# Kernel optimization log

Hardware: AMD Instinct MI355X
Metric: run time of the kernel (lower is better)

## Reference

```python
import jax, jax.numpy as jnp
import numpy as np

LN_EPS = 1e-3  # keras LayerNormalization default epsilon


def _layernorm(x, gamma, beta):
    mu = jnp.mean(x, axis=-1, keepdims=True)
    var = jnp.mean(jnp.square(x - mu), axis=-1, keepdims=True)
    return (x - mu) * jax.lax.rsqrt(var + LN_EPS) * gamma + beta


def setup_inputs() -> dict:
    key = jax.random.key(0)
    ks = jax.random.split(key, 8)
    B, H, W, C = 4, 64, 64, 256
    units = 256
    s = 1.0 / np.sqrt(C)  # he-normal-ish scale for 1x1 convs
    return {
        "inputs": jax.random.normal(ks[0], (B, H, W, C), jnp.float32),
        "context": jax.random.normal(ks[1], (B, H, W, C), jnp.float32),
        "Wq": jax.random.normal(ks[2], (C, units), jnp.float32) * s,
        "bq": jnp.zeros((units,), jnp.float32),
        "Wk": jax.random.normal(ks[3], (C, units), jnp.float32) * s,
        "bk": jnp.zeros((units,), jnp.float32),
        "Wv": jax.random.normal(ks[4], (C, units), jnp.float32) * s,
        "bv": jnp.zeros((units,), jnp.float32),
        "Wp": jax.random.normal(ks[5], (units, units), jnp.float32) * s,
        "bp": jnp.zeros((units,), jnp.float32),
        "gamma": jnp.ones((C,), jnp.float32),
        "beta": jnp.zeros((C,), jnp.float32),
    }


def reference(inputs, context, Wq, bq, Wk, bk, Wv, bv, Wp, bp, gamma, beta):
    B, H, W, C = inputs.shape
    units = Wq.shape[1]
    scale = jnp.float32(units) ** -0.5

    x_n = _layernorm(inputs, gamma, beta)          # normalized inputs (also residual base)
    q = jnp.einsum('bhwc,cu->bhwu', x_n, Wq) + bq   # [B,H,W,U]
    k = jnp.einsum('bhwc,cu->bhwu', context, Wk) + bk
    v = jnp.einsum('bhwc,cu->bhwu', context, Wv) + bv

    # full (h*w) x (H*W) score tensor, as in the original
    scores = jnp.einsum('bhwc,bHWc->bhwHW', q, k) * scale
    scores = scores.reshape(B, H, W, H * W)
    attn = jax.nn.softmax(scores, axis=-1).reshape(B, H, W, H, W)

    out = jnp.einsum('bhwHW,bHWc->bhwc', attn, v)
    proj = jnp.einsum('bhwc,cu->bhwu', out, Wp) + bp
    return x_n + proj
```

## Files before the change

kernel.cpp:

```cpp
#include <hip/hip_runtime.h>

typedef short v8s __attribute__((ext_vector_type(8)));
typedef float v4f __attribute__((ext_vector_type(4)));
using u16 = unsigned short;


__device__ __forceinline__ u16 f2b(float f) {
  union { float f; unsigned u; } v; v.f = f;
  unsigned r = v.u + 0x7FFFu + ((v.u >> 16) & 1u);
  return (u16)(r >> 16);
}

__global__ void ln_prep(const float* __restrict__ x, const float* __restrict__ ctx,
                        const float* __restrict__ gamma, const float* __restrict__ beta,
                        float* __restrict__ xn_f, u16* __restrict__ xn_b,
                        u16* __restrict__ ctx_b)
{
  const int tid = threadIdx.x;
  const int wid = tid >> 6, lane = tid & 63;
  const int row = blockIdx.x * 4 + wid;
  const size_t tidx = ((size_t)(row >> 4) * 8 + (lane >> 3)) * 512 +
                      (((lane >> 1) & 3) * 16 + (row & 15)) * 8 + (lane & 1) * 4;
  if (blockIdx.y == 0) {
    const float4 xv = *(const float4*)(x + (size_t)row * 256 + lane * 4);
    float s1 = xv.x + xv.y + xv.z + xv.w;
    float s2 = xv.x*xv.x + xv.y*xv.y + xv.z*xv.z + xv.w*xv.w;
#pragma unroll
    for (int m = 32; m >= 1; m >>= 1) {
      s1 += __shfl_xor(s1, m);
      s2 += __shfl_xor(s2, m);
    }
    const float mu  = s1 * (1.0f/256.0f);
    const float var = s2 * (1.0f/256.0f) - mu*mu;
    const float rs  = rsqrtf(var + 1e-3f);
    const float4 g = *(const float4*)(gamma + lane*4);
    const float4 b = *(const float4*)(beta  + lane*4);
    float4 y;
    y.x = (xv.x-mu)*rs*g.x + b.x;
    y.y = (xv.y-mu)*rs*g.y + b.y;
    y.z = (xv.z-mu)*rs*g.z + b.z;
    y.w = (xv.w-mu)*rs*g.w + b.w;
    *(float4*)(xn_f + (size_t)row*256 + lane*4) = y;
    ushort4 yb; yb.x=f2b(y.x); yb.y=f2b(y.y); yb.z=f2b(y.z); yb.w=f2b(y.w);
    *(ushort4*)(xn_b + tidx) = yb;
  } else {
    const float4 cv = *(const float4*)(ctx + (size_t)row * 256 + lane * 4);
    ushort4 cb; cb.x=f2b(cv.x); cb.y=f2b(cv.y); cb.z=f2b(cv.z); cb.w=f2b(cv.w);
    *(ushort4*)(ctx_b + tidx) = cb;
  }
}

__global__ void wtrans(const float* __restrict__ wq, const float* __restrict__ wk,
                       const float* __restrict__ wv, const float* __restrict__ wp,
                       u16* __restrict__ tq, u16* __restrict__ tk,
                       u16* __restrict__ tv, u16* __restrict__ tp)
{
  const float* src; u16* dst;
  switch (blockIdx.y) {
    case 0:  src = wq; dst = tq; break;
    case 1:  src = wk; dst = tk; break;
    case 2:  src = wv; dst = tv; break;
    default: src = wp; dst = tp; break;
  }
  const int t  = threadIdx.x;
  const int kk = blockIdx.x * 16 + (t >> 4);
  const int n0 = (t & 15) * 16;
  const size_t base = (size_t)((t & 15) * 8 + (kk >> 5)) * 512 +
                      ((kk >> 3) & 3) * 16 * 8 + (kk & 7);
#pragma unroll
  for (int j = 0; j < 16; j++)
    dst[base + (size_t)j * 8] = f2b(src[(size_t)kk * 256 + n0 + j]);
}

__global__ __launch_bounds__(256) void gemm_qkv(
    const u16* __restrict__ xn_b, const u16* __restrict__ ctx_b,
    const u16* __restrict__ wqt, const u16* __restrict__ wkt, const u16* __restrict__ wvt,
    const float* __restrict__ bq, const float* __restrict__ bk, const float* __restrict__ bv,
    u16* __restrict__ qo, u16* __restrict__ ko, u16* __restrict__ vto)
{
  const int mode = blockIdx.y;
  const u16* A; const u16* Wt; const float* bias;
  if (mode == 0)      { A = xn_b;  Wt = wqt; bias = bq; }
  else if (mode == 1) { A = ctx_b; Wt = wkt; bias = bk; }
  else                { A = ctx_b; Wt = wvt; bias = bv; }
  const int wid = threadIdx.x >> 6, lane = threadIdx.x & 63;
  const int lm = lane & 15, q4 = lane >> 4;
  const int m0 = blockIdx.x * 64 + wid * 16;
  const u16* abase = A + (size_t)(m0 >> 4) * 4096 + lane * 8;
  v8s af[8];
#pragma unroll
  for (int kf = 0; kf < 8; kf++) af[kf] = *(const v8s*)(abase + kf * 512);
#pragma unroll
  for (int ct = 0; ct < 16; ct++) {
    const int c = ct * 16 + lm;
    const u16* wbase = Wt + (size_t)ct * 4096 + lane * 8;
    v4f acc = {0.f, 0.f, 0.f, 0.f};
#pragma unroll
    for (int kf = 0; kf < 8; kf++)
      acc = __builtin_amdgcn_mfma_f32_16x16x32_bf16(af[kf], *(const v8s*)(wbase + kf * 512), acc, 0, 0, 0);
    const float bb = bias[c];
    if (mode == 2) {
      const int b = m0 >> 12;
      const int chunk = (m0 & 4095) >> 6;
      const int kic = (m0 & 63) + q4 * 4;
      const int ks = kic >> 5;
      const int q4p = (kic >> 3) & 3;
      const size_t idx = ((size_t)(b * 64 + chunk) * 32 + (c >> 4) * 2 + ks) * 512 +
                         (q4p * 16 + (c & 15)) * 8 + (q4 & 1) * 4;
      ushort4 pk;
      pk.x = f2b(acc[0] + bb); pk.y = f2b(acc[1] + bb);
      pk.z = f2b(acc[2] + bb); pk.w = f2b(acc[3] + bb);
      *(ushort4*)(vto + idx) = pk;
    } else {
      u16* out = (mode == 0) ? qo : ko;
      const size_t base = ((size_t)(m0 >> 4) * 8 + (c >> 5)) * 512 +
                          (((c >> 3) & 3) * 16 + q4 * 4) * 8 + (c & 7);
#pragma unroll
      for (int r = 0; r < 4; r++)
        out[base + (size_t)r * 8] = f2b(acc[r] + bb);
    }
  }
}

__global__ __launch_bounds__(256, 1) void attn_kernel(
    const u16* __restrict__ q, const u16* __restrict__ k,
    const u16* __restrict__ vt, u16* __restrict__ ao)
{
  __shared__ u16 P[2][64][72];
  __shared__ float Lp[4][64];
  __shared__ float Lt[64];
  const int b   = blockIdx.y;
  const int tid = threadIdx.x;
  const int w   = tid >> 6, lane = tid & 63;
  const int lm  = lane & 15, q4 = lane >> 4;
  const int m0  = blockIdx.x * 64;
  const u16* qb = q  + (size_t)b * 1048576;
  const u16* kb = k  + (size_t)b * 1048576;
  const u16* vb = vt + (size_t)b * 1048576;

  v8s qf[4][8];
#pragma unroll
  for (int qt = 0; qt < 4; qt++) {
    const u16* qbase = qb + (size_t)((m0 >> 4) + qt) * 4096 + lane * 8;
#pragma unroll
    for (int kf = 0; kf < 8; kf++) qf[qt][kf] = *(const v8s*)(qbase + kf * 512);
  }

  v4f o[4][4];
#pragma unroll
  for (int qt = 0; qt < 4; qt++)
#pragma unroll
    for (int ct = 0; ct < 4; ct++) o[qt][ct] = (v4f){0.f, 0.f, 0.f, 0.f};
  float lsum[4] = {0.f, 0.f, 0.f, 0.f};

  v8s kfr[8];
  {
    const u16* kbase = kb + (size_t)(w) * 4096 + lane * 8;
#pragma unroll
    for (int kf = 0; kf < 8; kf++) kfr[kf] = *(const v8s*)(kbase + kf * 512);
  }

  for (int s0 = 0; s0 < 4096; s0 += 64) {
    const int pb = (s0 >> 6) & 1;
    const int chunk = s0 >> 6;
    v8s vfr[4][2];
#pragma unroll
    for (int ct = 0; ct < 4; ct++) {
      const u16* vbase = vb + ((size_t)chunk * 32 + (w * 4 + ct) * 2) * 512 + lane * 8;
      vfr[ct][0] = *(const v8s*)(vbase);
      vfr[ct][1] = *(const v8s*)(vbase + 512);
    }
    v4f sc[4];
#pragma unroll
    for (int qt = 0; qt < 4; qt++) sc[qt] = (v4f){0.f, 0.f, 0.f, 0.f};
#pragma unroll
    for (int kf = 0; kf < 8; kf++)
#pragma unroll
      for (int qt = 0; qt < 4; qt++)
        sc[qt] = __builtin_amdgcn_mfma_f32_16x16x32_bf16(kfr[kf], qf[qt][kf], sc[qt], 0, 0, 0);
    {
      const int sn = (s0 + 64) & 4095;
      const u16* kbase = kb + (size_t)((sn >> 4) + w) * 4096 + lane * 8;
#pragma unroll
      for (int kf = 0; kf < 8; kf++) kfr[kf] = *(const v8s*)(kbase + kf * 512);
    }
#pragma unroll
    for (int qt = 0; qt < 4; qt++) {
      const float e0 = exp2f(sc[qt][0] * 0.09016844f);
      const float e1 = exp2f(sc[qt][1] * 0.09016844f);
      const float e2 = exp2f(sc[qt][2] * 0.09016844f);
      const float e3 = exp2f(sc[qt][3] * 0.09016844f);
      lsum[qt] += (e0 + e1) + (e2 + e3);
      unsigned d0, d1;
      asm("v_cvt_pk_bf16_f32 %0, %1, %2" : "=v"(d0) : "v"(e0), "v"(e1));
      asm("v_cvt_pk_bf16_f32 %0, %1, %2" : "=v"(d1) : "v"(e2), "v"(e3));
      uint2 pk; pk.x = d0; pk.y = d1;
      *(uint2*)(&P[pb][qt * 16 + lm][w * 16 + q4 * 4]) = pk;
    }
    __syncthreads();
#pragma unroll
    for (int qt = 0; qt < 4; qt++) {
      const v8s pf0 = *(const v8s*)(&P[pb][qt * 16 + lm][q4 * 8]);
      const v8s pf1 = *(const v8s*)(&P[pb][qt * 16 + lm][32 + q4 * 8]);
#pragma unroll
      for (int ct = 0; ct < 4; ct++) {
        o[qt][ct] = __builtin_amdgcn_mfma_f32_16x16x32_bf16(pf0, vfr[ct][0], o[qt][ct], 0, 0, 0);
        o[qt][ct] = __builtin_amdgcn_mfma_f32_16x16x32_bf16(pf1, vfr[ct][1], o[qt][ct], 0, 0, 0);
      }
    }
  }

#pragma unroll
  for (int qt = 0; qt < 4; qt++) {
    float t = lsum[qt];
    t += __shfl_xor(t, 16);
    t += __shfl_xor(t, 32);
    lsum[qt] = t;
  }
  if (q4 == 0) {
#pragma unroll
    for (int qt = 0; qt < 4; qt++) Lp[w][qt * 16 + lm] = lsum[qt];
  }
  __syncthreads();
  if (tid < 64) Lt[tid] = Lp[0][tid] + Lp[1][tid] + Lp[2][tid] + Lp[3][tid];
  __syncthreads();

  const int rstrip0 = (b * 4096 + m0) >> 4;
#pragma unroll
  for (int qt = 0; qt < 4; qt++)
#pragma unroll
    for (int r = 0; r < 4; r++) {
      const float linv = 1.0f / Lt[qt * 16 + q4 * 4 + r];
#pragma unroll
      for (int ct = 0; ct < 4; ct++) {
        const int ch = w * 64 + ct * 16 + lm;
        const size_t idx = ((size_t)(rstrip0 + qt) * 8 + (ch >> 5)) * 512 +
                           (((ch >> 3) & 3) * 16 + q4 * 4 + r) * 8 + (ch & 7);
        ao[idx] = f2b(o[qt][ct][r] * linv);
      }
    }
}

__global__ __launch_bounds__(256) void gemm_proj(
    const u16* __restrict__ A, const u16* __restrict__ Wt, const float* __restrict__ bias,
    const float* __restrict__ xn_f, float* __restrict__ out)
{
  const int wid = threadIdx.x >> 6, lane = threadIdx.x & 63;
  const int lm = lane & 15, q4 = lane >> 4;
  const int m0 = blockIdx.x * 64 + wid * 16;
  const u16* abase = A + (size_t)(m0 >> 4) * 4096 + lane * 8;
  v8s af[8];
#pragma unroll
  for (int kf = 0; kf < 8; kf++) af[kf] = *(const v8s*)(abase + kf * 512);
#pragma unroll
  for (int ct = 0; ct < 16; ct++) {
    const int c = ct * 16 + lm;
    const u16* wbase = Wt + (size_t)ct * 4096 + lane * 8;
    v4f acc = {0.f, 0.f, 0.f, 0.f};
#pragma unroll
    for (int kf = 0; kf < 8; kf++)
      acc = __builtin_amdgcn_mfma_f32_16x16x32_bf16(af[kf], *(const v8s*)(wbase + kf * 512), acc, 0, 0, 0);
    const float bb = bias[c];
#pragma unroll
    for (int r = 0; r < 4; r++) {
      const size_t idx = (size_t)(m0 + q4 * 4 + r) * 256 + c;
      out[idx] = xn_f[idx] + acc[r] + bb;
    }
  }
}

extern "C" void kernel_launch(void* const* d_in, const int* in_sizes, int n_in,
                              void* d_out, int out_size, void* d_ws, size_t ws_size,
                              hipStream_t stream)
{
  (void)in_sizes; (void)n_in; (void)out_size; (void)ws_size;
  const float* inputs  = (const float*)d_in[0];
  const float* context = (const float*)d_in[1];
  const float* Wq = (const float*)d_in[2];
  const float* bq = (const float*)d_in[3];
  const float* Wk = (const float*)d_in[4];
  const float* bk = (const float*)d_in[5];
  const float* Wv = (const float*)d_in[6];
  const float* bv = (const float*)d_in[7];
  const float* Wp = (const float*)d_in[8];
  const float* bp = (const float*)d_in[9];
  const float* gamma = (const float*)d_in[10];
  const float* beta  = (const float*)d_in[11];
  float* out = (float*)d_out;

  char* p = (char*)d_ws;
  float* xn_f = (float*)p; p += (size_t)16384 * 256 * 4;
  u16* xn_b   = (u16*)p;   p += (size_t)16384 * 256 * 2;
  u16* ctx_b  = (u16*)p;   p += (size_t)16384 * 256 * 2;
  u16* qbuf   = (u16*)p;   p += (size_t)16384 * 256 * 2;
  u16* kbuf   = (u16*)p;   p += (size_t)16384 * 256 * 2;
  u16* vtbuf  = (u16*)p;   p += (size_t)16384 * 256 * 2;
  u16* wqt = (u16*)p; p += (size_t)256 * 256 * 2;
  u16* wkt = (u16*)p; p += (size_t)256 * 256 * 2;
  u16* wvt = (u16*)p; p += (size_t)256 * 256 * 2;
  u16* wpt = (u16*)p; p += (size_t)256 * 256 * 2;
  u16* aobuf = xn_b;

  ln_prep<<<dim3(4096, 2), 256, 0, stream>>>(inputs, context, gamma, beta, xn_f, xn_b, ctx_b);
  wtrans<<<dim3(16, 4), 256, 0, stream>>>(Wq, Wk, Wv, Wp, wqt, wkt, wvt, wpt);
  gemm_qkv<<<dim3(256, 3), 256, 0, stream>>>(xn_b, ctx_b, wqt, wkt, wvt, bq, bk, bv, qbuf, kbuf, vtbuf);
  attn_kernel<<<dim3(64, 4), 256, 0, stream>>>(qbuf, kbuf, vtbuf, aobuf);
  gemm_proj<<<dim3(256), 256, 0, stream>>>(aobuf, wpt, bp, xn_f, out);
}
```

Baseline: 248.3 us.

## Fold softmax scale into Wq, retile QKV/proj GEMMs, remap attention blocks

Folds the softmax scale (with log2e) into the Q weight and bias, so the attention loop no longer multiplies each score before exp2. The QKV and projection GEMMs are retiled so each wave computes 64 rows and reuses each loaded weight fragment across four row tiles, using 128-thread blocks. The attention grid is flattened and blocks are interleaved across batches, which may change L2 locality for K/V. The __syncthreads in the attention loop is replaced with an explicit LDS waitcnt plus s_barrier. Rounding Q after scaling changes numerics slightly, and the wider per-wave tiles raise register pressure.

```diff
diff --git a/kernel.cpp b/kernel.cpp
--- a/kernel.cpp
+++ b/kernel.cpp
@@ -4,6 +4,7 @@
 typedef float v4f __attribute__((ext_vector_type(4)));
 using u16 = unsigned short;
 
+#define QSCALE 0.09016844f
 
 __device__ __forceinline__ u16 f2b(float f) {
   union { float f; unsigned u; } v; v.f = f;
@@ -55,9 +56,9 @@
                        u16* __restrict__ tq, u16* __restrict__ tk,
                        u16* __restrict__ tv, u16* __restrict__ tp)
 {
-  const float* src; u16* dst;
+  const float* src; u16* dst; float scl = 1.0f;
   switch (blockIdx.y) {
-    case 0:  src = wq; dst = tq; break;
+    case 0:  src = wq; dst = tq; scl = QSCALE; break;
     case 1:  src = wk; dst = tk; break;
     case 2:  src = wv; dst = tv; break;
     default: src = wp; dst = tp; break;
@@ -69,10 +70,10 @@
                       ((kk >> 3) & 3) * 16 * 8 + (kk & 7);
 #pragma unroll
   for (int j = 0; j < 16; j++)
-    dst[base + (size_t)j * 8] = f2b(src[(size_t)kk * 256 + n0 + j]);
-}
-
-__global__ __launch_bounds__(256) void gemm_qkv(
+    dst[base + (size_t)j * 8] = f2b(src[(size_t)kk * 256 + n0 + j] * scl);
+}
+
+__global__ __launch_bounds__(128) void gemm_qkv(
     const u16* __restrict__ xn_b, const u16* __restrict__ ctx_b,
     const u16* __restrict__ wqt, const u16* __restrict__ wkt, const u16* __restrict__ wvt,
     const float* __restrict__ bq, const float* __restrict__ bk, const float* __restrict__ bv,
@@ -83,41 +84,56 @@
   if (mode == 0)      { A = xn_b;  Wt = wqt; bias = bq; }
   else if (mode == 1) { A = ctx_b; Wt = wkt; bias = bk; }
   else                { A = ctx_b; Wt = wvt; bias = bv; }
+  const float bscale = (mode == 0) ? QSCALE : 1.0f;
   const int wid = threadIdx.x >> 6, lane = threadIdx.x & 63;
   const int lm = lane & 15, q4 = lane >> 4;
-  const int m0 = blockIdx.x * 64 + wid * 16;
-  const u16* abase = A + (size_t)(m0 >> 4) * 4096 + lane * 8;
-  v8s af[8];
-#pragma unroll
-  for (int kf = 0; kf < 8; kf++) af[kf] = *(const v8s*)(abase + kf * 512);
+  const int m0 = blockIdx.x * 128 + wid * 64;
+  v8s af[4][8];
+#pragma unroll
+  for (int rt = 0; rt < 4; rt++) {
+    const u16* abase = A + (size_t)((m0 >> 4) + rt) * 4096 + lane * 8;
+#pragma unroll
+    for (int kf = 0; kf < 8; kf++) af[rt][kf] = *(const v8s*)(abase + kf * 512);
+  }
 #pragma unroll
   for (int ct = 0; ct < 16; ct++) {
     const int c = ct * 16 + lm;
     const u16* wbase = Wt + (size_t)ct * 4096 + lane * 8;
-    v4f acc = {0.f, 0.f, 0.f, 0.f};
+    v8s wf[8];
+#pragma unroll
+    for (int kf = 0; kf < 8; kf++) wf[kf] = *(const v8s*)(wbase + kf * 512);
+    v4f acc[4];
+#pragma unroll
+    for (int rt = 0; rt < 4; rt++) acc[rt] = (v4f){0.f, 0.f, 0.f, 0.f};
 #pragma unroll
     for (int kf = 0; kf < 8; kf++)
-      acc = __builtin_amdgcn_mfma_f32_16x16x32_bf16(af[kf], *(const v8s*)(wbase + kf * 512), acc, 0, 0, 0);
-    const float bb = bias[c];
-    if (mode == 2) {
-      const int b = m0 >> 12;
-      const int chunk = (m0 & 4095) >> 6;
-      const int kic = (m0 & 63) + q4 * 4;
-      const int ks = kic >> 5;
-      const int q4p = (kic >> 3) & 3;
-      const size_t idx = ((size_t)(b * 64 + chunk) * 32 + (c >> 4) * 2 + ks) * 512 +
-                         (q4p * 16 + (c & 15)) * 8 + (q4 & 1) * 4;
-      ushort4 pk;
-      pk.x = f2b(acc[0] + bb); pk.y = f2b(acc[1] + bb);
-      pk.z = f2b(acc[2] + bb); pk.w = f2b(acc[3] + bb);
-      *(ushort4*)(vto + idx) = pk;
-    } else {
-      u16* out = (mode == 0) ? qo : ko;
-      const size_t base = ((size_t)(m0 >> 4) * 8 + (c >> 5)) * 512 +
-                          (((c >> 3) & 3) * 16 + q4 * 4) * 8 + (c & 7);
-#pragma unroll
-      for (int r = 0; r < 4; r++)
-        out[base + (size_t)r * 8] = f2b(acc[r] + bb);
+#pragma unroll
+      for (int rt = 0; rt < 4; rt++)
+        acc[rt] = __builtin_amdgcn_mfma_f32_16x16x32_bf16(af[rt][kf], wf[kf], acc[rt], 0, 0, 0);
+    const float bb = bias[c] * bscale;
+#pragma unroll
+    for (int rt = 0; rt < 4; rt++) {
+      const int row16 = m0 + rt * 16;
+      if (mode == 2) {
+        const int b = row16 >> 12;
+        const int chunk = (row16 & 4095) >> 6;
+        const int kic = (row16 & 63) + q4 * 4;
+        const int ks = kic >> 5;
+        const int q4p = (kic >> 3) & 3;
+        const size_t idx = ((size_t)(b * 64 + chunk) * 32 + (c >> 4) * 2 + ks) * 512 +
+                           (q4p * 16 + (c & 15)) * 8 + (q4 & 1) * 4;
+        ushort4 pk;
+        pk.x = f2b(acc[rt][0] + bb); pk.y = f2b(acc[rt][1] + bb);
+        pk.z = f2b(acc[rt][2] + bb); pk.w = f2b(acc[rt][3] + bb);
+        *(ushort4*)(vto + idx) = pk;
+      } else {
+        u16* out = (mode == 0) ? qo : ko;
+        const size_t base = ((size_t)(row16 >> 4) * 8 + (c >> 5)) * 512 +
+                            (((c >> 3) & 3) * 16 + q4 * 4) * 8 + (c & 7);
+#pragma unroll
+        for (int r = 0; r < 4; r++)
+          out[base + (size_t)r * 8] = f2b(acc[rt][r] + bb);
+      }
     }
   }
 }
@@ -129,11 +145,13 @@
   __shared__ u16 P[2][64][72];
   __shared__ float Lp[4][64];
   __shared__ float Lt[64];
-  const int b   = blockIdx.y;
+  const int bid  = blockIdx.x;
+  const int b    = (bid & 7) >> 1;
+  const int qblk = ((bid >> 3) << 1) | (bid & 1);
   const int tid = threadIdx.x;
   const int w   = tid >> 6, lane = tid & 63;
   const int lm  = lane & 15, q4 = lane >> 4;
-  const int m0  = blockIdx.x * 64;
+  const int m0  = qblk * 64;
   const u16* qb = q  + (size_t)b * 1048576;
   const u16* kb = k  + (size_t)b * 1048576;
   const u16* vb = vt + (size_t)b * 1048576;
@@ -155,7 +173,7 @@
 
   v8s kfr[8];
   {
-    const u16* kbase = kb + (size_t)(w) * 4096 + lane * 8;
+    const u16* kbase = kb + (size_t)w * 4096 + lane * 8;
 #pragma unroll
     for (int kf = 0; kf < 8; kf++) kfr[kf] = *(const v8s*)(kbase + kf * 512);
   }
@@ -186,10 +204,10 @@
     }
 #pragma unroll
     for (int qt = 0; qt < 4; qt++) {
-      const float e0 = exp2f(sc[qt][0] * 0.09016844f);
-      const float e1 = exp2f(sc[qt][1] * 0.09016844f);
-      const float e2 = exp2f(sc[qt][2] * 0.09016844f);
-      const float e3 = exp2f(sc[qt][3] * 0.09016844f);
+      const float e0 = exp2f(sc[qt][0]);
+      const float e1 = exp2f(sc[qt][1]);
+      const float e2 = exp2f(sc[qt][2]);
+      const float e3 = exp2f(sc[qt][3]);
       lsum[qt] += (e0 + e1) + (e2 + e3);
       unsigned d0, d1;
       asm("v_cvt_pk_bf16_f32 %0, %1, %2" : "=v"(d0) : "v"(e0), "v"(e1));
@@ -197,7 +215,8 @@
       uint2 pk; pk.x = d0; pk.y = d1;
       *(uint2*)(&P[pb][qt * 16 + lm][w * 16 + q4 * 4]) = pk;
     }
-    __syncthreads();
+    asm volatile("s_waitcnt lgkmcnt(0)" ::: "memory");
+    __builtin_amdgcn_s_barrier();
 #pragma unroll
     for (int qt = 0; qt < 4; qt++) {
       const v8s pf0 = *(const v8s*)(&P[pb][qt * 16 + lm][q4 * 8]);
@@ -241,31 +260,43 @@
     }
 }
 
-__global__ __launch_bounds__(256) void gemm_proj(
+__global__ __launch_bounds__(128) void gemm_proj(
     const u16* __restrict__ A, const u16* __restrict__ Wt, const float* __restrict__ bias,
     const float* __restrict__ xn_f, float* __restrict__ out)
 {
   const int wid = threadIdx.x >> 6, lane = threadIdx.x & 63;
   const int lm = lane & 15, q4 = lane >> 4;
-  const int m0 = blockIdx.x * 64 + wid * 16;
-  const u16* abase = A + (size_t)(m0 >> 4) * 4096 + lane * 8;
-  v8s af[8];
-#pragma unroll
-  for (int kf = 0; kf < 8; kf++) af[kf] = *(const v8s*)(abase + kf * 512);
+  const int m0 = blockIdx.x * 128 + wid * 64;
+  v8s af[4][8];
+#pragma unroll
+  for (int rt = 0; rt < 4; rt++) {
+    const u16* abase = A + (size_t)((m0 >> 4) + rt) * 4096 + lane * 8;
+#pragma unroll
+    for (int kf = 0; kf < 8; kf++) af[rt][kf] = *(const v8s*)(abase + kf * 512);
+  }
 #pragma unroll
   for (int ct = 0; ct < 16; ct++) {
     const int c = ct * 16 + lm;
     const u16* wbase = Wt + (size_t)ct * 4096 + lane * 8;
-    v4f acc = {0.f, 0.f, 0.f, 0.f};
+    v8s wf[8];
+#pragma unroll
+    for (int kf = 0; kf < 8; kf++) wf[kf] = *(const v8s*)(wbase + kf * 512);
+    v4f acc[4];
+#pragma unroll
+    for (int rt = 0; rt < 4; rt++) acc[rt] = (v4f){0.f, 0.f, 0.f, 0.f};
 #pragma unroll
     for (int kf = 0; kf < 8; kf++)
-      acc = __builtin_amdgcn_mfma_f32_16x16x32_bf16(af[kf], *(const v8s*)(wbase + kf * 512), acc, 0, 0, 0);
+#pragma unroll
+      for (int rt = 0; rt < 4; rt++)
+        acc[rt] = __builtin_amdgcn_mfma_f32_16x16x32_bf16(af[rt][kf], wf[kf], acc[rt], 0, 0, 0);
     const float bb = bias[c];
 #pragma unroll
-    for (int r = 0; r < 4; r++) {
-      const size_t idx = (size_t)(m0 + q4 * 4 + r) * 256 + c;
-      out[idx] = xn_f[idx] + acc[r] + bb;
-    }
+    for (int rt = 0; rt < 4; rt++)
+#pragma unroll
+      for (int r = 0; r < 4; r++) {
+        const size_t idx = (size_t)(m0 + rt * 16 + q4 * 4 + r) * 256 + c;
+        out[idx] = xn_f[idx] + acc[rt][r] + bb;
+      }
   }
 }
 
@@ -303,7 +334,7 @@
 
   ln_prep<<<dim3(4096, 2), 256, 0, stream>>>(inputs, context, gamma, beta, xn_f, xn_b, ctx_b);
   wtrans<<<dim3(16, 4), 256, 0, stream>>>(Wq, Wk, Wv, Wp, wqt, wkt, wvt, wpt);
-  gemm_qkv<<<dim3(256, 3), 256, 0, stream>>>(xn_b, ctx_b, wqt, wkt, wvt, bq, bk, bv, qbuf, kbuf, vtbuf);
-  attn_kernel<<<dim3(64, 4), 256, 0, stream>>>(qbuf, kbuf, vtbuf, aobuf);
-  gemm_proj<<<dim3(256), 256, 0, stream>>>(aobuf, wpt, bp, xn_f, out);
-}
+  gemm_qkv<<<dim3(128, 3), 128, 0, stream>>>(xn_b, ctx_b, wqt, wkt, wvt, bq, bk, bv, qbuf, kbuf, vtbuf);
+  attn_kernel<<<dim3(256), 256, 0, stream>>>(qbuf, kbuf, vtbuf, aobuf);
+  gemm_proj<<<dim3(128), 128, 0, stream>>>(aobuf, wpt, bp, xn_f, out);
+}
```

Measured after the change: 273.1 us. +10.0%, slower.
